# Optimization experiments

Hardware: AMD Instinct MI355X
Metric: run time of the kernel (lower is better)

The kernel has to match this reference:

```python
import jax, jax.numpy as jnp
import numpy as np

WIN = 11          # win_size
NC = 2            # num_classes
SMOOTH = 0.1      # smoothing / (num_classes - 1) = 0.1/1; fix_flag=True and 0.1 <= Max_Smootning=0.2


def setup_inputs() -> dict:
    key = jax.random.key(0)
    k1, k2 = jax.random.split(key)
    x = jax.random.normal(k1, (8, 2, 1024, 1024), dtype=jnp.float32)
    target = jax.random.randint(k2, (8, 1, 1024, 1024), 0, 2, dtype=jnp.int32)
    return {"x": x, "target": target}


def reference(x, target):
    kern = -jnp.ones((1, 1, WIN, WIN), dtype=jnp.float32)
    kern = kern.at[0, 0, WIN // 2, WIN // 2].set(float(WIN * WIN - 1))

    tf = target.astype(jnp.float32)  # [B,1,H,W]
    pad = WIN // 2
    edge = jax.lax.conv_general_dilated(tf, kern, window_strides=(1, 1),
                                        padding=[(pad, pad), (pad, pad)])
    edge = jnp.where(edge != 0, 1.0, 0.0)  # [B,1,H,W], 1 near label edges

    log_p = jax.nn.log_softmax(x, axis=1)  # [B,C,H,W]

    # One-hot masks (to_categorical with alpha=0 and alpha=smoothing).
    oh = jax.nn.one_hot(target[:, 0], NC, dtype=jnp.float32)  # [B,H,W,C]
    oh = jnp.transpose(oh, (0, 3, 1, 2))                      # [B,C,H,W]
    # alpha everywhere, 1 - alpha + alpha/NC at the true class
    soft = SMOOTH + oh * (1.0 - 2.0 * SMOOTH + SMOOTH / NC)

    mask = oh * (1.0 - edge) + soft * edge  # hard label off-edge, smoothed on-edge
    loss = jnp.mean(jnp.sum(mask * log_p, axis=1))
    return -loss
```

## Files before the change

kernel.cpp:

```cpp
#include <hip/hip_runtime.h>

#define HH 1024
#define WW 1024
#define BB 8
#define TILE 64
#define HALO 5
#define TROWS 74
#define TB    80
#define VP    65
#define NBLK  (16*16*8)

__global__ __launch_bounds__(256) void ls_main(const float* __restrict__ x,
                                               const int* __restrict__ tgt,
                                               float* __restrict__ partial) {
    __shared__ int   s_t[TROWS * (TB / 4)];
    __shared__ int   s_v[74 * VP];
    __shared__ float s_red[4];
    unsigned char* s_tb = (unsigned char*)s_t;

    const int tid = threadIdx.x;
    const int b  = blockIdx.z;
    const int ty = blockIdx.y * TILE;
    const int tx = blockIdx.x * TILE;
    const int ty0 = ty - HALO;

    const int row = tid >> 2;
    const int c0  = (tid & 3) << 4;
    const float* x0p = x + ((size_t)b * 2 + 0) * HH * WW + (size_t)(ty + row) * WW + tx + c0;
    const float* x1p = x + ((size_t)b * 2 + 1) * HH * WW + (size_t)(ty + row) * WW + tx + c0;
    float4 xv0[4], xv1[4];
#pragma unroll
    for (int q = 0; q < 4; ++q) xv0[q] = ((const float4*)x0p)[q];
#pragma unroll
    for (int q = 0; q < 4; ++q) xv1[q] = ((const float4*)x1p)[q];
    const float* f0 = (const float*)xv0;
    const float* f1 = (const float*)xv1;

    const int* tb_g = tgt + (size_t)b * HH * WW;

    for (int i = tid; i < TROWS * (TB / 4); i += 256) {
        int r  = i / (TB / 4);
        int ch = i - r * (TB / 4);
        int gy  = ty0 + r;
        int gx0 = tx - 8 + ch * 4;
        unsigned int pk = 0;
        if ((unsigned)gy < HH) {
            if (gx0 >= 0 && gx0 + 3 < WW) {
                int4 v = *(const int4*)(tb_g + (size_t)gy * WW + gx0);
                pk = (unsigned)v.x | ((unsigned)v.y << 8) |
                     ((unsigned)v.z << 16) | ((unsigned)v.w << 24);
            } else {
#pragma unroll
                for (int k = 0; k < 4; ++k) {
                    int gx = gx0 + k;
                    if ((unsigned)gx < WW)
                        pk |= ((unsigned)tb_g[(size_t)gy * WW + gx]) << (8 * k);
                }
            }
        }
        s_t[i] = (int)pk;
    }
    __syncthreads();

    for (int i = tid; i < 296; i += 256) {
        int cc = 3 + (i >> 2);
        int r0 = (i & 3) << 4;
        int V = 0;
#pragma unroll
        for (int k = 0; k < 11; ++k) V += s_tb[(r0 + k) * TB + cc];
        int base = (cc - 3) * VP;
        for (int r = r0; r < r0 + 16; ++r) {
            s_v[base + r] = V;
            if (r != r0 + 15) V += (int)s_tb[(r + 11) * TB + cc] - (int)s_tb[r * TB + cc];
        }
    }
    __syncthreads();

    int W = 0;
#pragma unroll
    for (int d = 0; d < 11; ++d) W += s_v[(c0 + d) * VP + row];

    const unsigned long long* tp =
        (const unsigned long long*)(s_tb + (row + HALO) * TB + c0 + 8);
    unsigned long long tlo = tp[0], thi = tp[1];

    float acc = 0.f;
#pragma unroll
    for (int jj = 0; jj < 16; ++jj) {
        int t = (int)((jj < 8 ? (tlo >> (8 * jj)) : (thi >> (8 * (jj - 8)))) & 1);
        bool edge = (121 * t != W);
        if (jj != 15)
            W += s_v[(c0 + jj + 11) * VP + row] - s_v[(c0 + jj) * VP + row];

        float a0 = f0[jj], a1 = f1[jj];
        float m   = fmaxf(a0, a1);
        float lse = m + __logf(1.0f + __expf(-fabsf(a0 - a1)));
        float lp0 = a0 - lse, lp1 = a1 - lse;
        float lpt = t ? lp1 : lp0;
        float lpo = t ? lp0 : lp1;
        acc += edge ? (0.95f * lpt + 0.1f * lpo) : lpt;
    }

#pragma unroll
    for (int off = 32; off > 0; off >>= 1) acc += __shfl_down(acc, off, 64);
    if ((tid & 63) == 0) s_red[tid >> 6] = acc;
    __syncthreads();
    if (tid == 0) {
        int bid = (blockIdx.z * gridDim.y + blockIdx.y) * gridDim.x + blockIdx.x;
        partial[bid] = s_red[0] + s_red[1] + s_red[2] + s_red[3];
    }
}

__global__ __launch_bounds__(256) void ls_final(const float* __restrict__ partial,
                                                float* __restrict__ out) {
    __shared__ double s_red[4];
    const int tid = threadIdx.x;
    double s = 0.0;
    for (int i = tid; i < NBLK; i += 256) s += (double)partial[i];
#pragma unroll
    for (int off = 32; off > 0; off >>= 1) s += __shfl_down(s, off, 64);
    if ((tid & 63) == 0) s_red[tid >> 6] = s;
    __syncthreads();
    if (tid == 0) {
        double total = s_red[0] + s_red[1] + s_red[2] + s_red[3];
        out[0] = (float)(-total * (1.0 / (8.0 * 1024.0 * 1024.0)));
    }
}

extern "C" void kernel_launch(void* const* d_in, const int* in_sizes, int n_in,
                              void* d_out, int out_size, void* d_ws, size_t ws_size,
                              hipStream_t stream) {
    const float* x  = (const float*)d_in[0];
    const int* tgt  = (const int*)d_in[1];
    float* partial  = (float*)d_ws;

    dim3 grid(WW / TILE, HH / TILE, BB);
    hipLaunchKernelGGL(ls_main, grid, dim3(256), 0, stream, x, tgt, partial);
    hipLaunchKernelGGL(ls_final, dim3(1), dim3(256), 0, stream, partial, (float*)d_out);
}
```

Measured before the change: 126.0 us.

## Pack vertical box sums as bytes in row-major shared memory for vector reads

Vertical window sums are now computed four columns at a time on packed byte words, with SIMD-within-register adds on packed int32 lanes. They are stored row-major as bytes, so each thread reads its 32 needed sums with two 16-byte LDS loads instead of many strided int loads. It also adds an occupancy hint to launch_bounds and empty asm barriers that force the global x loads to complete before the barrier. This relies on each byte sum staying within 11, so no carries cross lanes, and it lowers shared memory use and LDS traffic.

```diff
diff --git a/kernel.cpp b/kernel.cpp
--- a/kernel.cpp
+++ b/kernel.cpp
@@ -6,15 +6,15 @@
 #define TILE 64
 #define HALO 5
 #define TROWS 74
-#define TB    80
-#define VP    65
+#define TD    20
+#define SVP   80
 #define NBLK  (16*16*8)
 
-__global__ __launch_bounds__(256) void ls_main(const float* __restrict__ x,
-                                               const int* __restrict__ tgt,
-                                               float* __restrict__ partial) {
-    __shared__ int   s_t[TROWS * (TB / 4)];
-    __shared__ int   s_v[74 * VP];
+__global__ __launch_bounds__(256, 6) void ls_main(const float* __restrict__ x,
+                                                  const int* __restrict__ tgt,
+                                                  float* __restrict__ partial) {
+    __shared__ __align__(16) int s_t[TROWS * TD];
+    __shared__ __align__(16) unsigned char s_v[TILE * SVP];
     __shared__ float s_red[4];
     unsigned char* s_tb = (unsigned char*)s_t;
 
@@ -33,14 +33,12 @@
     for (int q = 0; q < 4; ++q) xv0[q] = ((const float4*)x0p)[q];
 #pragma unroll
     for (int q = 0; q < 4; ++q) xv1[q] = ((const float4*)x1p)[q];
-    const float* f0 = (const float*)xv0;
-    const float* f1 = (const float*)xv1;
 
     const int* tb_g = tgt + (size_t)b * HH * WW;
 
-    for (int i = tid; i < TROWS * (TB / 4); i += 256) {
-        int r  = i / (TB / 4);
-        int ch = i - r * (TB / 4);
+    for (int i = tid; i < TROWS * TD; i += 256) {
+        int r  = i / TD;
+        int ch = i - r * TD;
         int gy  = ty0 + r;
         int gx0 = tx - 8 + ch * 4;
         unsigned int pk = 0;
@@ -60,37 +58,49 @@
         }
         s_t[i] = (int)pk;
     }
+
+#pragma unroll
+    for (int q = 0; q < 4; ++q) {
+        asm volatile("" :: "v"(xv0[q].x), "v"(xv0[q].y), "v"(xv0[q].z), "v"(xv0[q].w));
+        asm volatile("" :: "v"(xv1[q].x), "v"(xv1[q].y), "v"(xv1[q].z), "v"(xv1[q].w));
+    }
     __syncthreads();
 
-    for (int i = tid; i < 296; i += 256) {
-        int cc = 3 + (i >> 2);
-        int r0 = (i & 3) << 4;
+    if (tid < 80) {
+        int ch = tid >> 2;
+        int r0 = (tid & 3) << 4;
         int V = 0;
 #pragma unroll
-        for (int k = 0; k < 11; ++k) V += s_tb[(r0 + k) * TB + cc];
-        int base = (cc - 3) * VP;
+        for (int k = 0; k < 11; ++k) V += s_t[(r0 + k) * TD + ch];
         for (int r = r0; r < r0 + 16; ++r) {
-            s_v[base + r] = V;
-            if (r != r0 + 15) V += (int)s_tb[(r + 11) * TB + cc] - (int)s_tb[r * TB + cc];
+            *(int*)(s_v + r * SVP + (ch << 2)) = V;
+            if (r != r0 + 15) V += s_t[(r + 11) * TD + ch] - s_t[r * TD + ch];
         }
     }
     __syncthreads();
 
+    uint4 va = *(const uint4*)(s_v + row * SVP + c0);
+    uint4 vb = *(const uint4*)(s_v + row * SVP + c0 + 16);
+    unsigned char vbytes[32];
+    *(uint4*)(vbytes)      = va;
+    *(uint4*)(vbytes + 16) = vb;
+
+    const unsigned long long* tp =
+        (const unsigned long long*)(s_tb + (row + HALO) * SVP + c0 + 8);
+    unsigned long long tlo = tp[0], thi = tp[1];
+
     int W = 0;
 #pragma unroll
-    for (int d = 0; d < 11; ++d) W += s_v[(c0 + d) * VP + row];
+    for (int i = 3; i <= 13; ++i) W += vbytes[i];
 
-    const unsigned long long* tp =
-        (const unsigned long long*)(s_tb + (row + HALO) * TB + c0 + 8);
-    unsigned long long tlo = tp[0], thi = tp[1];
-
+    const float* f0 = (const float*)xv0;
+    const float* f1 = (const float*)xv1;
     float acc = 0.f;
 #pragma unroll
     for (int jj = 0; jj < 16; ++jj) {
         int t = (int)((jj < 8 ? (tlo >> (8 * jj)) : (thi >> (8 * (jj - 8)))) & 1);
         bool edge = (121 * t != W);
-        if (jj != 15)
-            W += s_v[(c0 + jj + 11) * VP + row] - s_v[(c0 + jj) * VP + row];
+        if (jj != 15) W += (int)vbytes[jj + 14] - (int)vbytes[jj + 3];
 
         float a0 = f0[jj], a1 = f1[jj];
         float m   = fmaxf(a0, a1);
```

Result: faster. 122.6 us (-2.7%).
